# Kernel optimization log

Measured on AMD Instinct MI355X. Metric: run time of the kernel, lower is better.

The kernel has to match this reference:

```python
import jax, jax.numpy as jnp
import numpy as np

B, S, D, K = 4, 4096, 1024, 64

def setup_inputs() -> dict:
    key = jax.random.key(0)
    kx, kq, kk, kv, ko = jax.random.split(key, 5)
    scale = 1.0 / np.sqrt(D)
    return {
        "x": jax.random.normal(kx, (B, S, D), dtype=jnp.float32),
        "Wq": jax.random.uniform(kq, (K, D), dtype=jnp.float32, minval=-scale, maxval=scale),
        "Wk": jax.random.uniform(kk, (K, D), dtype=jnp.float32, minval=-scale, maxval=scale),
        "Wv": jax.random.uniform(kv, (K, D), dtype=jnp.float32, minval=-scale, maxval=scale),
        "Wo": jax.random.uniform(ko, (D, K), dtype=jnp.float32, minval=-1.0/np.sqrt(K), maxval=1.0/np.sqrt(K)),
    }

def reference(x, Wq, Wk, Wv, Wo):
    # projections: torch Linear(dim, key_dim, bias=False) -> x @ W.T
    Q = jax.nn.elu(x @ Wq.T) + 1.0          # [B,S,K]
    Kf = jax.nn.elu(x @ Wk.T) + 1.0         # [B,S,K]
    V = x @ Wv.T                             # [B,S,K]
    # causal running KV state via cumsum of outer products: [B,S,K,K]
    KV_sum = jnp.cumsum(Kf[..., :, None] * V[..., None, :], axis=1)
    K_sum = jnp.cumsum(Kf, axis=1)           # [B,S,K]
    num = jnp.einsum('bsk,bskm->bsm', Q, KV_sum)   # [B,S,K]
    den = jnp.einsum('bsk,bsk->bs', Q, K_sum)[..., None]
    out = num / (den + 1e-6)
    return out @ Wo.T                         # [B,S,D]
```

## Files before the change

### kernel.cpp

```cpp
#include <hip/hip_runtime.h>

#define BB 4
#define SS 4096
#define DDIM 1024
#define KDIM 64
#define NCHUNK 64
#define TCHUNK 256
#define MROWS 16384

typedef short short8v __attribute__((ext_vector_type(8)));
typedef float f32x4 __attribute__((ext_vector_type(4)));
#define MFMA16 __builtin_amdgcn_mfma_f32_16x16x32_bf16

__device__ __forceinline__ ushort f2bf(float f) {
    uint u = __float_as_uint(f);
    u += 0x7FFFu + ((u >> 16) & 1u);
    return (ushort)(u >> 16);
}

__global__ __launch_bounds__(256) void k_wconv(
    const float* __restrict__ Wq, const float* __restrict__ Wk,
    const float* __restrict__ Wv, const float* __restrict__ Wo,
    ushort* __restrict__ Whf, ushort* __restrict__ Wof)
{
    const int b = blockIdx.x, t = threadIdx.x;
    const int ks = t >> 7;
    const int l = (t >> 1) & 63;
    const int half = t & 1;
    if (b < 192) {
        const int s = b / 12, cf = b % 12;
        const int grow = cf * 16 + (l & 15);
        const int gcol = s * 64 + ks * 32 + ((l >> 4) & 3) * 8 + half * 4;
        const float* src = (grow < 64) ? (Wq + (size_t)grow * DDIM)
                         : (grow < 128) ? (Wk + (size_t)(grow - 64) * DDIM)
                                        : (Wv + (size_t)(grow - 128) * DDIM);
        float4 v = *(const float4*)&src[gcol];
        ushort* dst = &Whf[(size_t)(((s * 12 + cf) * 2 + ks) * 64 + l) * 8 + half * 4];
        dst[0] = f2bf(v.x); dst[1] = f2bf(v.y); dst[2] = f2bf(v.z); dst[3] = f2bf(v.w);
    } else {
        const int cf = b - 192;
        const int d = cf * 16 + (l & 15);
        const int kc = ks * 32 + ((l >> 4) & 3) * 8 + half * 4;
        float4 v = *(const float4*)&Wo[(size_t)d * KDIM + kc];
        ushort* dst = &Wof[(size_t)((cf * 2 + ks) * 64 + l) * 8 + half * 4];
        dst[0] = f2bf(v.x); dst[1] = f2bf(v.y); dst[2] = f2bf(v.z); dst[3] = f2bf(v.w);
    }
}

#define EBP 216
__global__ __launch_bounds__(512) void k_proj(
    const float* __restrict__ x, const ushort* __restrict__ Whf,
    ushort* __restrict__ Qf, ushort* __restrict__ Kff,
    ushort* __restrict__ KfT, ushort* __restrict__ VT)
{
    __shared__ ushort xs[64 * 512];
    const int t = threadIdx.x;
    const int w = t >> 6, l = t & 63;
    const int rw = w >> 2, cw = w & 3;
    const int mb = blockIdx.x;
    const int row0 = mb * 32;
    const int lq = l >> 4;

    {
#pragma unroll
        for (int i = 0; i < 8; ++i) {
            const int c8 = i * 512 + t;
            const int r = c8 >> 7;
            const int col = (c8 & 127) * 8;
            const float* p = &x[(size_t)(row0 + r) * DDIM + col];
            float4 u0 = *(const float4*)p;
            float4 u1 = *(const float4*)(p + 4);
            short8v hh;
            hh[0] = (short)f2bf(u0.x); hh[1] = (short)f2bf(u0.y);
            hh[2] = (short)f2bf(u0.z); hh[3] = (short)f2bf(u0.w);
            hh[4] = (short)f2bf(u1.x); hh[5] = (short)f2bf(u1.y);
            hh[6] = (short)f2bf(u1.z); hh[7] = (short)f2bf(u1.w);
            const int frag = (r >> 4) * 32 + (col >> 5);
            const int slot = ((r & 15) | (((col >> 3) & 3) << 4)) ^ (frag & 7);
            *(short8v*)&xs[(size_t)(frag * 64 + slot) * 8] = hh;
        }
    }
    __syncthreads();

    f32x4 acc[3];
#pragma unroll
    for (int c = 0; c < 3; ++c) acc[c] = (f32x4){0.f, 0.f, 0.f, 0.f};

    auto loadW = [&](int sg, short8v (&bw)[6]) {
#pragma unroll
        for (int j = 0; j < 6; ++j) {
            const int cf = cw * 3 + (j >> 1);
            const int f = cf * 2 + (j & 1);
            bw[j] = *(const short8v*)&Whf[((size_t)(sg * 24 + f)) * 512 + l * 8];
        }
    };
    auto computeStep = [&](int sl, short8v (&bw)[6]) {
#pragma unroll
        for (int ks = 0; ks < 2; ++ks) {
            const int f = rw * 32 + sl * 2 + ks;
            short8v a = *(const short8v*)&xs[(size_t)(f * 64 + (l ^ (f & 7))) * 8];
#pragma unroll
            for (int c = 0; c < 3; ++c)
                acc[c] = MFMA16(a, bw[c * 2 + ks], acc[c], 0, 0, 0);
        }
    };

    {
        short8v bwA[6], bwB[6];
        loadW(0, bwA);
        for (int s = 0; s < 16; s += 2) {
            loadW(s + 1, bwB);
            computeStep(s, bwA);
            if (s + 2 < 16) loadW(s + 2, bwA);
            computeStep(s + 1, bwB);
        }
    }

    __syncthreads();
    ushort* eb = xs;
#pragma unroll
    for (int ci = 0; ci < 3; ++ci) {
        const int col = (cw * 3 + ci) * 16 + (l & 15);
#pragma unroll
        for (int q = 0; q < 4; ++q) {
            const int row = rw * 16 + lq * 4 + q;
            float v = acc[ci][q];
            if (col < 128) v = (v > 0.f) ? v + 1.f : __expf(v);
            eb[row * EBP + col] = f2bf(v);
        }
    }
    __syncthreads();

    {
        const int fj = t >> 6;
        const int which = fj >> 2, rf = (fj >> 1) & 1, ks = fj & 1;
        const int r = rf * 16 + (l & 15);
        const int c0 = ks * 32 + ((l >> 4) & 3) * 8;
        const size_t fo = ((size_t)(mb * 4 + rf * 2 + ks)) * 512 + l * 8;
        if (which == 0) {
            short8v q8 = *(const short8v*)&eb[r * EBP + c0];
            *(short8v*)&Qf[fo] = q8;
        } else {
            short8v k8 = *(const short8v*)&eb[r * EBP + 64 + c0];
            *(short8v*)&Kff[fo] = k8;
        }
    }
    {
        const int fj = t >> 6;
        const int which = fj >> 2, f = fj & 3;
        const int col = (which ? 128 : 64) + f * 16 + (l & 15);
        const int jb = ((l >> 4) & 3) * 8;
        short8v tv;
#pragma unroll
        for (int e = 0; e < 8; ++e) tv[e] = (short)eb[(jb + e) * EBP + col];
        const size_t fo = ((size_t)((mb >> 1) * 8 + f * 2 + (mb & 1))) * 512 + l * 8;
        if (which == 0) *(short8v*)&KfT[fo] = tv;
        else            *(short8v*)&VT[fo]  = tv;
    }
}

__global__ __launch_bounds__(64) void k_chunksum(
    const ushort* __restrict__ KfT, const ushort* __restrict__ VT,
    float* __restrict__ KVc, float* __restrict__ Ksc)
{
    const int g = blockIdx.x, l = threadIdx.x;
    short8v ka[4][2], vb[4][2];
#pragma unroll
    for (int f = 0; f < 4; ++f)
#pragma unroll
        for (int js = 0; js < 2; ++js) {
            const size_t fo = ((size_t)(g * 8 + f * 2 + js)) * 512 + l * 8;
            ka[f][js] = *(const short8v*)&KfT[fo];
            vb[f][js] = *(const short8v*)&VT[fo];
        }
    short8v onesf;
#pragma unroll
    for (int e = 0; e < 8; ++e) onesf[e] = ((l & 15) == 0) ? (short)0x3F80 : (short)0;

    f32x4 acc[4][5];
#pragma unroll
    for (int kf = 0; kf < 4; ++kf)
#pragma unroll
        for (int mf = 0; mf < 5; ++mf) acc[kf][mf] = (f32x4){0.f, 0.f, 0.f, 0.f};
#pragma unroll
    for (int js = 0; js < 2; ++js)
#pragma unroll
        for (int kf = 0; kf < 4; ++kf) {
#pragma unroll
            for (int mf = 0; mf < 4; ++mf)
                acc[kf][mf] = MFMA16(ka[kf][js], vb[mf][js], acc[kf][mf], 0, 0, 0);
            acc[kf][4] = MFMA16(ka[kf][js], onesf, acc[kf][4], 0, 0, 0);
        }
    const int lq = l >> 4;
#pragma unroll
    for (int kf = 0; kf < 4; ++kf) {
#pragma unroll
        for (int q = 0; q < 4; ++q) {
            const int k = kf * 16 + lq * 4 + q;
#pragma unroll
            for (int mf = 0; mf < 4; ++mf)
                KVc[(size_t)g * 4096 + k * 64 + mf * 16 + (l & 15)] = acc[kf][mf][q];
            if ((l & 15) == 0) Ksc[(size_t)g * KDIM + k] = acc[kf][4][q];
        }
    }
}

__global__ void k_scan(const float* __restrict__ KVc, const float* __restrict__ Ksc,
                       float* __restrict__ Sst, float* __restrict__ Kss)
{
    const int b = blockIdx.x / 65;
    const int r = blockIdx.x % 65;
    const int t = threadIdx.x;
    if (r < 64) {
        const int e = r * 64 + t;
        float v[64];
#pragma unroll
        for (int i = 0; i < 64; ++i)
            v[i] = KVc[((size_t)(b * NCHUNK + i)) * 4096 + e];
        float acc = 0.f;
#pragma unroll
        for (int i = 0; i < 64; ++i) {
            Sst[((size_t)(b * NCHUNK + i)) * 4096 + e] = acc;
            acc += v[i];
        }
    } else {
        float v[64];
#pragma unroll
        for (int i = 0; i < 64; ++i)
            v[i] = Ksc[((size_t)(b * NCHUNK + i)) * KDIM + t];
        float acc = 0.f;
#pragma unroll
        for (int i = 0; i < 64; ++i) {
            Kss[((size_t)(b * NCHUNK + i)) * KDIM + t] = acc;
            acc += v[i];
        }
    }
}

__global__ __launch_bounds__(256) void k_intra(
    const ushort* __restrict__ Qf, const ushort* __restrict__ Kff,
    const ushort* __restrict__ VT, const float* __restrict__ Sst,
    const float* __restrict__ Kss, const ushort* __restrict__ Wof,
    float* __restrict__ out)
{
    __shared__ ushort pb[32 * 64];
    __shared__ ushort sT[80 * 64];
    __shared__ float ob[4][16 * 68 + 4];
    const int bx = blockIdx.x, t = threadIdx.x;
    const int g = bx >> 1, rh = bx & 1;
    const int w = t >> 6, l = t & 63;
    const int lq = l >> 4;

    {
        const int k = t >> 2, m0 = (t & 3) * 16;
        const float4* sp = (const float4*)&Sst[(size_t)g * 4096 + k * 64 + m0];
        float4 f0 = sp[0], f1 = sp[1], f2v = sp[2], f3 = sp[3];
        float fv[16] = {f0.x, f0.y, f0.z, f0.w, f1.x, f1.y, f1.z, f1.w,
                        f2v.x, f2v.y, f2v.z, f2v.w, f3.x, f3.y, f3.z, f3.w};
#pragma unroll
        for (int i = 0; i < 16; ++i) {
            const int m = m0 + i;
            sT[m * 64 + (k ^ ((m & 7) << 3))] = f2bf(fv[i]);
        }
        if (t < 64) sT[64 * 64 + t] = f2bf(Kss[(size_t)g * KDIM + t]);
        for (int idx = t; idx < 960; idx += 256) sT[65 * 64 + idx] = 0;
    }

    const int rf = w & 1;
    short8v qa[2];
#pragma unroll
    for (int ks = 0; ks < 2; ++ks)
        qa[ks] = *(const short8v*)&Qf[((size_t)((g * 2 + rh) * 4 + rf * 2 + ks)) * 512 + l * 8];
    {
        const int cfh = w >> 1;
        f32x4 accs[2];
#pragma unroll
        for (int ci = 0; ci < 2; ++ci) accs[ci] = (f32x4){0.f, 0.f, 0.f, 0.f};
#pragma unroll
        for (int ci = 0; ci < 2; ++ci) {
            const int cf = cfh * 2 + ci;
#pragma unroll
            for (int ks = 0; ks < 2; ++ks) {
                short8v kb = *(const short8v*)&Kff[((size_t)((g * 2 + (cf >> 1)) * 4 + (cf & 1) * 2 + ks)) * 512 + l * 8];
                accs[ci] = MFMA16(qa[ks], kb, accs[ci], 0, 0, 0);
            }
        }
#pragma unroll
        for (int ci = 0; ci < 2; ++ci)
#pragma unroll
            for (int q = 0; q < 4; ++q) {
                const int row = rf * 16 + lq * 4 + q;
                const int col = (cfh * 2 + ci) * 16 + (l & 15);
                const float sv = (col <= rh * 32 + row) ? accs[ci][q] : 0.f;
                pb[row * 64 + (col ^ ((row & 7) << 3))] = f2bf(sv);
            }
    }
    __syncthreads();

    const int mg = w >> 1;
    f32x4 an0 = (f32x4){0.f,0.f,0.f,0.f}, an1 = (f32x4){0.f,0.f,0.f,0.f};
    f32x4 ad = (f32x4){0.f,0.f,0.f,0.f};
    short8v onesf;
#pragma unroll
    for (int e = 0; e < 8; ++e) onesf[e] = ((l & 15) == 0) ? (short)0x3F80 : (short)0;
#pragma unroll
    for (int js = 0; js < 2; ++js) {
        const int prow = rf * 16 + (l & 15);
        const int pbase = js * 32 + ((l >> 4) & 3) * 8;
        short8v pa = *(const short8v*)&pb[prow * 64 + (pbase ^ ((prow & 7) << 3))];
        short8v v0 = *(const short8v*)&VT[((size_t)(g * 8 + (mg * 2 + 0) * 2 + js)) * 512 + l * 8];
        short8v v1 = *(const short8v*)&VT[((size_t)(g * 8 + (mg * 2 + 1) * 2 + js)) * 512 + l * 8];
        an0 = MFMA16(pa, v0, an0, 0, 0, 0);
        an1 = MFMA16(pa, v1, an1, 0, 0, 0);
        ad  = MFMA16(pa, onesf, ad, 0, 0, 0);
    }
#pragma unroll
    for (int ks = 0; ks < 2; ++ks) {
        const int base = ks * 32 + ((l >> 4) & 3) * 8;
        const int r0 = (mg * 2 + 0) * 16 + (l & 15);
        const int r1 = (mg * 2 + 1) * 16 + (l & 15);
        const int r4 = 64 + (l & 15);
        short8v s0 = *(const short8v*)&sT[r0 * 64 + (base ^ ((r0 & 7) << 3))];
        short8v s1 = *(const short8v*)&sT[r1 * 64 + (base ^ ((r1 & 7) << 3))];
        short8v s4 = *(const short8v*)&sT[r4 * 64 + (base ^ ((r4 & 7) << 3))];
        an0 = MFMA16(qa[ks], s0, an0, 0, 0, 0);
        an1 = MFMA16(qa[ks], s1, an1, 0, 0, 0);
        ad  = MFMA16(qa[ks], s4, ad, 0, 0, 0);
    }
#pragma unroll
    for (int q = 0; q < 4; ++q) {
        const float den = __shfl(ad[q], (l & 48));
        const float rinv = 1.f / (den + 1e-6f);
        const int row = rf * 16 + lq * 4 + q;
        const int c0 = (mg * 2 + 0) * 16 + (l & 15);
        const int c1 = (mg * 2 + 1) * 16 + (l & 15);
        pb[row * 64 + (c0 ^ ((row & 7) << 3))] = f2bf(an0[q] * rinv);
        pb[row * 64 + (c1 ^ ((row & 7) << 3))] = f2bf(an1[q] * rinv);
    }
    __syncthreads();

    short8v oa[2][2];
#pragma unroll
    for (int rfi = 0; rfi < 2; ++rfi)
#pragma unroll
        for (int ks = 0; ks < 2; ++ks) {
            const int row = rfi * 16 + (l & 15);
            const int base = ks * 32 + ((l >> 4) & 3) * 8;
            oa[rfi][ks] = *(const short8v*)&pb[row * 64 + (base ^ ((row & 7) << 3))];
        }
    float* obw = ob[w];
#pragma unroll
    for (int rr = 0; rr < 4; ++rr) {
        f32x4 acco[2][4];
#pragma unroll
        for (int rfi = 0; rfi < 2; ++rfi)
#pragma unroll
            for (int ci = 0; ci < 4; ++ci) acco[rfi][ci] = (f32x4){0.f, 0.f, 0.f, 0.f};
#pragma unroll
        for (int ci = 0; ci < 4; ++ci) {
            const int cfg = w * 16 + rr * 4 + ci;
#pragma unroll
            for (int ks = 0; ks < 2; ++ks) {
                short8v wb = *(const short8v*)&Wof[((size_t)(cfg * 2 + ks)) * 512 + l * 8];
#pragma unroll
                for (int rfi = 0; rfi < 2; ++rfi)
                    acco[rfi][ci] = MFMA16(oa[rfi][ks], wb, acco[rfi][ci], 0, 0, 0);
            }
        }
#pragma unroll
        for (int rfi = 0; rfi < 2; ++rfi) {
#pragma unroll
            for (int ci = 0; ci < 4; ++ci)
#pragma unroll
                for (int q = 0; q < 4; ++q)
                    obw[(lq * 4 + q) * 68 + ci * 16 + (l & 15)] = acco[rfi][ci][q];
#pragma unroll
            for (int rg = 0; rg < 4; ++rg) {
                const int row = rg * 4 + lq;
                float4 vv = *(const float4*)&obw[row * 68 + (l & 15) * 4];
                *(float4*)&out[((size_t)(g * 64 + rh * 32 + rfi * 16 + row)) * DDIM
                               + w * 256 + rr * 64 + (l & 15) * 4] = vv;
            }
        }
    }
}

extern "C" void kernel_launch(void* const* d_in, const int* in_sizes, int n_in,
                              void* d_out, int out_size, void* d_ws, size_t ws_size,
                              hipStream_t stream)
{
    const float* x  = (const float*)d_in[0];
    const float* Wq = (const float*)d_in[1];
    const float* Wk = (const float*)d_in[2];
    const float* Wv = (const float*)d_in[3];
    const float* Wo = (const float*)d_in[4];
    float* out = (float*)d_out;

    float* ws   = (float*)d_ws;
    float* KVc  = ws;
    float* Sst  = KVc + (size_t)TCHUNK * 4096;
    float* Ksc  = Sst + (size_t)TCHUNK * 4096;
    float* Kss  = Ksc + (size_t)TCHUNK * KDIM;
    ushort* Whf = (ushort*)(Kss + (size_t)TCHUNK * KDIM);
    ushort* Wof = Whf + (size_t)192 * DDIM;
    ushort* Qf  = Wof + (size_t)64 * 1024;
    ushort* Kff = Qf  + (size_t)512 * 4 * 512;
    ushort* KfT = Kff + (size_t)512 * 4 * 512;
    ushort* VT  = KfT + (size_t)256 * 8 * 512;

    k_wconv<<<dim3(256), dim3(256), 0, stream>>>(Wq, Wk, Wv, Wo, Whf, Wof);
    k_proj<<<dim3(MROWS / 32), dim3(512), 0, stream>>>(x, Whf, Qf, Kff, KfT, VT);
    k_chunksum<<<dim3(TCHUNK), dim3(64), 0, stream>>>(KfT, VT, KVc, Ksc);
    k_scan<<<dim3(BB * 65), dim3(64), 0, stream>>>(KVc, Ksc, Sst, Kss);
    k_intra<<<dim3(TCHUNK * 2), dim3(256), 0, stream>>>(Qf, Kff, VT, Sst, Kss, Wof, out);
}
```

Baseline: 57.97 us.

## Pipeline k_proj with async global-to-LDS loads and 64-row tiles

Rewrites the projection kernel so each block handles 64 rows instead of 32. Per K-step slices of fp32 x and bf16 weights are streamed into double-buffered LDS with global_load_lds, and x is converted to bf16 with a packed convert just before the MFMAs. This overlaps the memory traffic with compute, drops the upfront full-row staging, and reuses each weight fragment across two row tiles. In exchange the grid shrinks to 256 blocks, there is a barrier on every K-step, and the LDS footprint changes, which could lower occupancy.

```diff
diff --git a/kernel.cpp b/kernel.cpp
--- a/kernel.cpp
+++ b/kernel.cpp
@@ -12,10 +12,20 @@
 typedef float f32x4 __attribute__((ext_vector_type(4)));
 #define MFMA16 __builtin_amdgcn_mfma_f32_16x16x32_bf16
 
+#define GLDS16(gp, lp) __builtin_amdgcn_global_load_lds( \
+    (const __attribute__((address_space(1))) unsigned int*)(gp), \
+    (__attribute__((address_space(3))) unsigned int*)(lp), 16, 0, 0)
+
 __device__ __forceinline__ ushort f2bf(float f) {
     uint u = __float_as_uint(f);
     u += 0x7FFFu + ((u >> 16) & 1u);
     return (ushort)(u >> 16);
+}
+
+__device__ __forceinline__ uint cvtpk(float lo, float hi) {
+    uint r;
+    asm("v_cvt_pk_bf16_f32 %0, %1, %2" : "=v"(r) : "v"(lo), "v"(hi));
+    return r;
 }
 
 __global__ __launch_bounds__(256) void k_wconv(
@@ -48,114 +58,120 @@
 }
 
 #define EBP 216
-__global__ __launch_bounds__(512) void k_proj(
+__global__ __launch_bounds__(512, 2) void k_proj(
     const float* __restrict__ x, const ushort* __restrict__ Whf,
     ushort* __restrict__ Qf, ushort* __restrict__ Kff,
     ushort* __restrict__ KfT, ushort* __restrict__ VT)
 {
-    __shared__ ushort xs[64 * 512];
+    __shared__ float  ldsA[2][4096];
+    __shared__ ushort ldsB[2][12288];
     const int t = threadIdx.x;
     const int w = t >> 6, l = t & 63;
     const int rw = w >> 2, cw = w & 3;
-    const int mb = blockIdx.x;
-    const int row0 = mb * 32;
+    const int g = blockIdx.x;
+    const int row0 = g * 64;
     const int lq = l >> 4;
 
+    auto stageX = [&](int s, int buf) {
+#pragma unroll
+        for (int ii = 0; ii < 2; ++ii) {
+            const int i = w * 2 + ii;
+            const int r = 4 * i + (l >> 4);
+            const int sg = ((l & 15) >> 1) ^ (r & 7);
+            const float* gp = &x[(size_t)(row0 + r) * DDIM + s * 64 + sg * 8 + (l & 1) * 4];
+            GLDS16(gp, &ldsA[buf][i * 256]);
+        }
+    };
+    auto stageW = [&](int s, int buf) {
+#pragma unroll
+        for (int ii = 0; ii < 3; ++ii) {
+            const int f = w * 3 + ii;
+            const ushort* gp = &Whf[(size_t)(s * 24 + f) * 512 + l * 8];
+            GLDS16(gp, &ldsB[buf][f * 512]);
+        }
+    };
+
+    f32x4 acc[2][3];
+#pragma unroll
+    for (int r = 0; r < 2; ++r)
+#pragma unroll
+        for (int c = 0; c < 3; ++c) acc[r][c] = (f32x4){0.f, 0.f, 0.f, 0.f};
+
+    auto compute = [&](int buf) {
+#pragma unroll
+        for (int ks = 0; ks < 2; ++ks) {
+            short8v a[2];
+#pragma unroll
+            for (int j = 0; j < 2; ++j) {
+                const int r = (rw * 2 + j) * 16 + (l & 15);
+                const int gs = (ks * 4 + (l >> 4)) ^ (l & 7);
+                const float* ap = &ldsA[buf][r * 64 + gs * 8];
+                float4 a0 = *(const float4*)ap;
+                float4 a1 = *(const float4*)(ap + 4);
+                uint4 pk;
+                pk.x = cvtpk(a0.x, a0.y); pk.y = cvtpk(a0.z, a0.w);
+                pk.z = cvtpk(a1.x, a1.y); pk.w = cvtpk(a1.z, a1.w);
+                a[j] = *(short8v*)&pk;
+            }
+#pragma unroll
+            for (int c = 0; c < 3; ++c) {
+                short8v b = *(const short8v*)&ldsB[buf][(size_t)((cw * 3 + c) * 2 + ks) * 512 + l * 8];
+                acc[0][c] = MFMA16(a[0], b, acc[0][c], 0, 0, 0);
+                acc[1][c] = MFMA16(a[1], b, acc[1][c], 0, 0, 0);
+            }
+        }
+    };
+
+    stageX(0, 0); stageW(0, 0);
+    __syncthreads();
+    for (int s = 0; s < 16; ++s) {
+        const int cur = s & 1, nxt = cur ^ 1;
+        if (s < 15) { stageX(s + 1, nxt); stageW(s + 1, nxt); }
+        compute(cur);
+        __syncthreads();
+    }
+
+    ushort* eb = (ushort*)&ldsA[0][0];
+#pragma unroll
+    for (int rfi = 0; rfi < 2; ++rfi)
+#pragma unroll
+        for (int ci = 0; ci < 3; ++ci) {
+            const int col = (cw * 3 + ci) * 16 + (l & 15);
+#pragma unroll
+            for (int q = 0; q < 4; ++q) {
+                const int rl = (rw * 2 + rfi) * 16 + lq * 4 + q;
+                float v = acc[rfi][ci][q];
+                if (col < 128) v = (v > 0.f) ? v + 1.f : __expf(v);
+                eb[rl * EBP + col] = f2bf(v);
+            }
+        }
+    __syncthreads();
+
     {
-#pragma unroll
-        for (int i = 0; i < 8; ++i) {
-            const int c8 = i * 512 + t;
-            const int r = c8 >> 7;
-            const int col = (c8 & 127) * 8;
-            const float* p = &x[(size_t)(row0 + r) * DDIM + col];
-            float4 u0 = *(const float4*)p;
-            float4 u1 = *(const float4*)(p + 4);
-            short8v hh;
-            hh[0] = (short)f2bf(u0.x); hh[1] = (short)f2bf(u0.y);
-            hh[2] = (short)f2bf(u0.z); hh[3] = (short)f2bf(u0.w);
-            hh[4] = (short)f2bf(u1.x); hh[5] = (short)f2bf(u1.y);
-            hh[6] = (short)f2bf(u1.z); hh[7] = (short)f2bf(u1.w);
-            const int frag = (r >> 4) * 32 + (col >> 5);
-            const int slot = ((r & 15) | (((col >> 3) & 3) << 4)) ^ (frag & 7);
-            *(short8v*)&xs[(size_t)(frag * 64 + slot) * 8] = hh;
-        }
-    }
-    __syncthreads();
-
-    f32x4 acc[3];
-#pragma unroll
-    for (int c = 0; c < 3; ++c) acc[c] = (f32x4){0.f, 0.f, 0.f, 0.f};
-
-    auto loadW = [&](int sg, short8v (&bw)[6]) {
-#pragma unroll
-        for (int j = 0; j < 6; ++j) {
-            const int cf = cw * 3 + (j >> 1);
-            const int f = cf * 2 + (j & 1);
-            bw[j] = *(const short8v*)&Whf[((size_t)(sg * 24 + f)) * 512 + l * 8];
-        }
-    };
-    auto computeStep = [&](int sl, short8v (&bw)[6]) {
+        const int which = w >> 2, rh = (w >> 1) & 1, rfm = w & 1;
 #pragma unroll
         for (int ks = 0; ks < 2; ++ks) {
-            const int f = rw * 32 + sl * 2 + ks;
-            short8v a = *(const short8v*)&xs[(size_t)(f * 64 + (l ^ (f & 7))) * 8];
-#pragma unroll
-            for (int c = 0; c < 3; ++c)
-                acc[c] = MFMA16(a, bw[c * 2 + ks], acc[c], 0, 0, 0);
-        }
-    };
-
+            const int r = rh * 32 + rfm * 16 + (l & 15);
+            const int c0 = ks * 32 + ((l >> 4) & 3) * 8 + (which ? 64 : 0);
+            short8v v8 = *(const short8v*)&eb[r * EBP + c0];
+            const size_t fo = ((size_t)((g * 2 + rh) * 4 + rfm * 2 + ks)) * 512 + l * 8;
+            if (which == 0) *(short8v*)&Qf[fo] = v8;
+            else            *(short8v*)&Kff[fo] = v8;
+        }
+    }
     {
-        short8v bwA[6], bwB[6];
-        loadW(0, bwA);
-        for (int s = 0; s < 16; s += 2) {
-            loadW(s + 1, bwB);
-            computeStep(s, bwA);
-            if (s + 2 < 16) loadW(s + 2, bwA);
-            computeStep(s + 1, bwB);
-        }
-    }
-
-    __syncthreads();
-    ushort* eb = xs;
-#pragma unroll
-    for (int ci = 0; ci < 3; ++ci) {
-        const int col = (cw * 3 + ci) * 16 + (l & 15);
-#pragma unroll
-        for (int q = 0; q < 4; ++q) {
-            const int row = rw * 16 + lq * 4 + q;
-            float v = acc[ci][q];
-            if (col < 128) v = (v > 0.f) ? v + 1.f : __expf(v);
-            eb[row * EBP + col] = f2bf(v);
-        }
-    }
-    __syncthreads();
-
-    {
-        const int fj = t >> 6;
-        const int which = fj >> 2, rf = (fj >> 1) & 1, ks = fj & 1;
-        const int r = rf * 16 + (l & 15);
-        const int c0 = ks * 32 + ((l >> 4) & 3) * 8;
-        const size_t fo = ((size_t)(mb * 4 + rf * 2 + ks)) * 512 + l * 8;
-        if (which == 0) {
-            short8v q8 = *(const short8v*)&eb[r * EBP + c0];
-            *(short8v*)&Qf[fo] = q8;
-        } else {
-            short8v k8 = *(const short8v*)&eb[r * EBP + 64 + c0];
-            *(short8v*)&Kff[fo] = k8;
-        }
-    }
-    {
-        const int fj = t >> 6;
-        const int which = fj >> 2, f = fj & 3;
-        const int col = (which ? 128 : 64) + f * 16 + (l & 15);
-        const int jb = ((l >> 4) & 3) * 8;
-        short8v tv;
-#pragma unroll
-        for (int e = 0; e < 8; ++e) tv[e] = (short)eb[(jb + e) * EBP + col];
-        const size_t fo = ((size_t)((mb >> 1) * 8 + f * 2 + (mb & 1))) * 512 + l * 8;
-        if (which == 0) *(short8v*)&KfT[fo] = tv;
-        else            *(short8v*)&VT[fo]  = tv;
+        const int which = w >> 2, f = w & 3;
+#pragma unroll
+        for (int js = 0; js < 2; ++js) {
+            const int col = (which ? 128 : 64) + f * 16 + (l & 15);
+            const int jb = js * 32 + ((l >> 4) & 3) * 8;
+            short8v tv;
+#pragma unroll
+            for (int e = 0; e < 8; ++e) tv[e] = (short)eb[(jb + e) * EBP + col];
+            const size_t fo = ((size_t)(g * 8 + f * 2 + js)) * 512 + l * 8;
+            if (which == 0) *(short8v*)&KfT[fo] = tv;
+            else            *(short8v*)&VT[fo]  = tv;
+        }
     }
 }
 
@@ -409,7 +425,7 @@
     ushort* VT  = KfT + (size_t)256 * 8 * 512;
 
     k_wconv<<<dim3(256), dim3(256), 0, stream>>>(Wq, Wk, Wv, Wo, Whf, Wof);
-    k_proj<<<dim3(MROWS / 32), dim3(512), 0, stream>>>(x, Whf, Qf, Kff, KfT, VT);
+    k_proj<<<dim3(TCHUNK), dim3(512), 0, stream>>>(x, Whf, Qf, Kff, KfT, VT);
     k_chunksum<<<dim3(TCHUNK), dim3(64), 0, stream>>>(KfT, VT, KVc, Ksc);
     k_scan<<<dim3(BB * 65), dim3(64), 0, stream>>>(KVc, Ksc, Sst, Kss);
     k_intra<<<dim3(TCHUNK * 2), dim3(256), 0, stream>>>(Qf, Kff, VT, Sst, Kss, Wof, out);
```

Result: faster. 56.20 us (-3.1%).
